# Kernel optimization log

Hardware: AMD Instinct MI355X
Metric: run time of the kernel (lower is better)

Reference implementation:

```python
import jax, jax.numpy as jnp
import numpy as np

TEMPERATURE = 0.1
NEG_FILL = -9e15


def setup_inputs() -> dict:
    key = jax.random.key(0)
    k1, k2, k3, k4 = jax.random.split(key, 4)
    N, D = 2048, 256
    loc1 = jax.random.normal(k1, (N, D), dtype=jnp.float32)
    loc2 = jax.random.normal(k3, (N, D), dtype=jnp.float32)
    # variances must be positive; sample in [0.5, 1.5)
    scale1 = jax.random.uniform(k2, (N, D), dtype=jnp.float32, minval=0.5, maxval=1.5)
    scale2 = jax.random.uniform(k4, (N, D), dtype=jnp.float32, minval=0.5, maxval=1.5)
    return {"loc1": loc1, "scale1": scale1, "loc2": loc2, "scale2": scale2}


def _kl_loss(loc1, scale1, loc2, scale2):
    N, D = loc1.shape
    mu = jnp.concatenate([loc1, loc2], axis=0)    # [2N, D]
    var = jnp.concatenate([scale1, scale2], axis=0)  # [2N, D] (treated as variance)
    inv_var = 1.0 / var
    s_logvar = jnp.sum(jnp.log(var), axis=-1)      # [2N]
    # kld[i,j] = 0.5 * sum_d( logvar_j - logvar_i - 1 + ((mu_i-mu_j)^2 + var_i)/var_j )
    # expand (mu_i-mu_j)^2 = mu_i^2 - 2 mu_i mu_j + mu_j^2 -> three GEMM/reduction terms
    a = (mu * mu + var) @ inv_var.T                # [2N,2N]: sum_d (mu_i^2+var_i)/var_j
    b = mu @ (mu * inv_var).T                      # [2N,2N]: sum_d mu_i mu_j / var_j
    c = jnp.sum(mu * mu * inv_var, axis=-1)        # [2N]:    sum_d mu_j^2 / var_j
    kld = 0.5 * (s_logvar[None, :] - s_logvar[:, None]
                 - jnp.float32(D) + a - 2.0 * b + c[None, :])
    M = 2 * N
    idx = jnp.arange(M)
    kld = kld.at[idx, idx].set(NEG_FILL)           # fill_diagonal_(-9e15)
    sim = kld / TEMPERATURE
    pos = sim[idx, (idx - N) % M]                  # eye rolled by N along dim 0
    loss = jax.nn.logsumexp(sim, axis=-1) - pos
    return jnp.mean(loss)


def reference(loc1, scale1, loc2, scale2):
    return _kl_loss(loc1, scale1, loc2, scale2)
```

## Files before the change

kernel.cpp:

```cpp
#include <hip/hip_runtime.h>
#include <hip/hip_bf16.h>
#include <math.h>

#define N_HALF 2048
#define M_TOT  4096
#define D_DIM  256
#define K2     512
#define NBLK   16
#define NKT    16
#define A_TB   8192
#define B_TB   16384
#define BUF_B  24576
#define NROWB  32

typedef __attribute__((ext_vector_type(8))) short bf16x8;
typedef __attribute__((ext_vector_type(4))) float f32x4;

static __device__ __forceinline__ unsigned short f2bf(float x) {
    union { __hip_bfloat16 h; unsigned short u; } cv;
    cv.h = __float2bfloat16(x);
    return cv.u;
}

static __device__ __forceinline__ void gll16(const void* g, void* l) {
    __builtin_amdgcn_global_load_lds(
        (const __attribute__((address_space(1))) unsigned int*)g,
        (__attribute__((address_space(3))) unsigned int*)l, 16, 0, 0);
}

#define FENCE asm volatile("" ::: "memory")
#define BAR() do { FENCE; __builtin_amdgcn_s_barrier(); FENCE; } while (0)
#define VM(n) asm volatile("s_waitcnt vmcnt(" #n ")" ::: "memory")

__global__ __launch_bounds__(256) void prep_kernel(
        const float* __restrict__ loc1, const float* __restrict__ scale1,
        const float* __restrict__ loc2, const float* __restrict__ scale2,
        unsigned short* __restrict__ Ab, unsigned short* __restrict__ Bb,
        float* __restrict__ slv, float* __restrict__ cvec,
        float* __restrict__ out) {
    const int t = threadIdx.x, w = t >> 6, lane = t & 63;
    if (blockIdx.x == 0 && t == 0) out[0] = 0.0f;
    const int i = blockIdx.x * 4 + w;
    const float* mup  = (i < N_HALF) ? loc1 + (size_t)i * D_DIM   : loc2 + (size_t)(i - N_HALF) * D_DIM;
    const float* vap  = (i < N_HALF) ? scale1 + (size_t)i * D_DIM : scale2 + (size_t)(i - N_HALF) * D_DIM;
    const float4 mu = *(const float4*)(mup + lane * 4);
    const float4 va = *(const float4*)(vap + lane * 4);
    const float4 iv = {1.0f / va.x, 1.0f / va.y, 1.0f / va.z, 1.0f / va.w};

    float lacc = __logf(va.x * va.y * va.z * va.w);
    float cacc = mu.x * mu.x * iv.x + mu.y * mu.y * iv.y
               + mu.z * mu.z * iv.z + mu.w * mu.w * iv.w;
    #pragma unroll
    for (int off = 1; off < 64; off <<= 1) {
        lacc += __shfl_xor(lacc, off, 64);
        cacc += __shfl_xor(cacc, off, 64);
    }
    if (lane == 0) { slv[i] = lacc; cvec[i] = cacc; }

    const int rsw = (i >> 1) & 3;
    char* const abase = (char*)Ab + (size_t)(i >> 7) * (NKT * A_TB) + (i & 127) * 64;
    char* const bbase = (char*)Bb + (size_t)(i >> 8) * (NKT * B_TB) + (i & 255) * 64;
    #define ST4(base, TB, k, v0, v1, v2, v3)                                         \
        {   const int kk = (k);                                                      \
            const int kt = kk >> 5;                                                  \
            const int sl = ((kk >> 3) & 3) ^ rsw, hf = (kk >> 2) & 1;                \
            ushort4 pk = {f2bf(v0), f2bf(v1), f2bf(v2), f2bf(v3)};                   \
            *(ushort4*)((base) + (size_t)kt * (TB) + sl * 16 + hf * 8) = pk; }
    ST4(abase, A_TB, lane * 4,       mu.x * mu.x + va.x, mu.y * mu.y + va.y,
                                     mu.z * mu.z + va.z, mu.w * mu.w + va.w)
    ST4(abase, A_TB, 256 + lane * 4, -2.0f * mu.x, -2.0f * mu.y, -2.0f * mu.z, -2.0f * mu.w)
    ST4(bbase, B_TB, lane * 4,       iv.x, iv.y, iv.z, iv.w)
    ST4(bbase, B_TB, 256 + lane * 4, mu.x * iv.x, mu.y * iv.y, mu.z * iv.z, mu.w * iv.w)
    #undef ST4
}

__global__ __launch_bounds__(512, 4) void gemm_lse_kernel(
        const unsigned short* __restrict__ Ab, const unsigned short* __restrict__ Bb,
        const float* __restrict__ slv, const float* __restrict__ cvec,
        float* __restrict__ pm, float* __restrict__ ps,
        float* __restrict__ pos) {
    extern __shared__ __align__(16) char smem[];
    const int t = threadIdx.x;
    const int lane = t & 63, wid = t >> 6;
    const int bid = blockIdx.x;
    const int xcd = bid & 7, idx = bid >> 3;
    const int by2 = (xcd >> 1) * 8 + (idx >> 3);
    const int bx  = (xcd & 1) * 8 + (idx & 7);
    const int wrow = wid >> 2, wcol = wid & 3;
    const int fr = lane & 15, g = lane >> 4;
    const int t16 = t * 16;

    int a_off[4], b_off[4];
    #pragma unroll
    for (int fm = 0; fm < 4; ++fm) {
        const int row = wrow * 64 + fm * 16 + fr;
        a_off[fm] = row * 64 + ((g ^ ((row >> 1) & 3)) << 4);
    }
    #pragma unroll
    for (int fn = 0; fn < 4; ++fn) {
        const int row = wcol * 64 + fn * 16 + fr;
        b_off[fn] = 8192 + row * 64 + ((g ^ ((row >> 1) & 3)) << 4);
    }

    f32x4 acc[4][4];
    #pragma unroll
    for (int i = 0; i < 4; ++i)
        #pragma unroll
        for (int j = 0; j < 4; ++j) acc[i][j] = (f32x4){0.f, 0.f, 0.f, 0.f};

    const char* gA = (const char*)Ab + (size_t)by2 * (NKT * A_TB);
    const char* gB = (const char*)Bb + (size_t)bx * (NKT * B_TB);

    #define STAGE(ktile, bidx)                                                       \
        {   const char* _sA = gA + (size_t)(ktile) * A_TB;                           \
            const char* _sB = gB + (size_t)(ktile) * B_TB;                           \
            char* _d = smem + (bidx) * BUF_B;                                        \
            gll16(_sA + t16,        _d + t16);                                       \
            gll16(_sB + t16,        _d + 8192 + t16);                                \
            gll16(_sB + 8192 + t16, _d + 16384 + t16); }

    STAGE(0, 0)
    STAGE(1, 1)
    VM(3);
    BAR();

    int cur = 0;
    bf16x8 bfr[4], af[4];
    for (int kt = 0; kt < NKT; ++kt) {
        const char* bufc = smem + cur * BUF_B;
        int stg = cur + 2; if (stg >= 3) stg -= 3;
        if (kt + 2 < NKT) STAGE(kt + 2, stg)
        #pragma unroll
        for (int q = 0; q < 4; ++q) bfr[q] = *(const bf16x8*)(bufc + b_off[q]);
        #pragma unroll
        for (int q = 0; q < 4; ++q) af[q]  = *(const bf16x8*)(bufc + a_off[q]);
        __builtin_amdgcn_s_setprio(1);
        #pragma unroll
        for (int fm = 0; fm < 4; ++fm) {
            acc[fm][0] = __builtin_amdgcn_mfma_f32_16x16x32_bf16(af[fm], bfr[0], acc[fm][0], 0, 0, 0);
            acc[fm][1] = __builtin_amdgcn_mfma_f32_16x16x32_bf16(af[fm], bfr[1], acc[fm][1], 0, 0, 0);
            acc[fm][2] = __builtin_amdgcn_mfma_f32_16x16x32_bf16(af[fm], bfr[2], acc[fm][2], 0, 0, 0);
            acc[fm][3] = __builtin_amdgcn_mfma_f32_16x16x32_bf16(af[fm], bfr[3], acc[fm][3], 0, 0, 0);
        }
        __builtin_amdgcn_s_setprio(0);
        if (kt + 2 < NKT)       { VM(3); }
        else if (kt == NKT - 2) { VM(0); }
        BAR();
        cur = (cur + 1 == 3) ? 0 : cur + 1;
    }
    #undef STAGE

    float colv[4]; int gcol[4];
    #pragma unroll
    for (int fn = 0; fn < 4; ++fn) {
        const int c = bx * 256 + wcol * 64 + fn * 16 + fr;
        gcol[fn] = c;
        colv[fn] = 5.0f * (slv[c] + cvec[c]) - 1280.0f;
    }
    float* redm = (float*)smem;
    float* reds = (float*)(smem + 2048);

    #pragma unroll
    for (int fm = 0; fm < 4; ++fm) {
        #pragma unroll
        for (int q = 0; q < 4; ++q) {
            const int rloc = wrow * 64 + fm * 16 + g * 4 + q;
            const int grow = by2 * 128 + rloc;
            const int jpart = grow ^ N_HALF;
            float v[4];
            #pragma unroll
            for (int fn = 0; fn < 4; ++fn) {
                const float x = 5.0f * acc[fm][fn][q] + colv[fn];
                if (gcol[fn] == jpart) pos[grow] = x;
                v[fn] = (grow == gcol[fn]) ? -3.0e38f : x;
            }
            float m = fmaxf(fmaxf(v[0], v[1]), fmaxf(v[2], v[3]));
            #pragma unroll
            for (int off = 1; off < 16; off <<= 1) m = fmaxf(m, __shfl_xor(m, off, 64));
            float s = __expf(v[0] - m) + __expf(v[1] - m) + __expf(v[2] - m) + __expf(v[3] - m);
            #pragma unroll
            for (int off = 1; off < 16; off <<= 1) s += __shfl_xor(s, off, 64);
            if (fr == 0) { redm[rloc * 4 + wcol] = m; reds[rloc * 4 + wcol] = s; }
        }
    }
    __syncthreads();
    if (t < 128) {
        float m = redm[t * 4], s = reds[t * 4];
        #pragma unroll
        for (int k = 1; k < 4; ++k) {
            const float mk = redm[t * 4 + k], sk = reds[t * 4 + k];
            const float nm = fmaxf(m, mk);
            s = s * __expf(m - nm) + sk * __expf(mk - nm);
            m = nm;
        }
        pm[(size_t)(by2 * 128 + t) * NBLK + bx] = m;
        ps[(size_t)(by2 * 128 + t) * NBLK + bx] = s;
    }
}

__global__ __launch_bounds__(256) void finalize_kernel(
        const float* __restrict__ pm, const float* __restrict__ ps,
        const float* __restrict__ pos, float* __restrict__ out) {
    __shared__ float sm[256];
    const int t = threadIdx.x;
    const int i = blockIdx.x * 256 + t;
    float mk[NBLK];
    float m = -3.0e38f;
    #pragma unroll
    for (int k = 0; k < NBLK; ++k) {
        mk[k] = pm[(size_t)i * NBLK + k];
        m = fmaxf(m, mk[k]);
    }
    float s = 0.0f;
    #pragma unroll
    for (int k = 0; k < NBLK; ++k)
        s += ps[(size_t)i * NBLK + k] * __expf(mk[k] - m);
    sm[t] = m + logf(s) - pos[i];
    __syncthreads();
    for (int off = 128; off > 0; off >>= 1) {
        if (t < off) sm[t] += sm[t + off];
        __syncthreads();
    }
    if (t == 0) atomicAdd(out, sm[0] * (1.0f / (float)M_TOT));
}

extern "C" void kernel_launch(void* const* d_in, const int* in_sizes, int n_in,
                              void* d_out, int out_size, void* d_ws, size_t ws_size,
                              hipStream_t stream) {
    const float* loc1   = (const float*)d_in[0];
    const float* scale1 = (const float*)d_in[1];
    const float* loc2   = (const float*)d_in[2];
    const float* scale2 = (const float*)d_in[3];
    float* out = (float*)d_out;

    char* ws = (char*)d_ws;
    unsigned short* Ab = (unsigned short*)ws;
    unsigned short* Bb = (unsigned short*)(ws + (size_t)4 * 1024 * 1024);
    float* slv  = (float*)(ws + (size_t)8 * 1024 * 1024);
    float* cvec = slv + M_TOT;
    float* pm   = cvec + M_TOT;
    float* ps   = pm + (size_t)M_TOT * NBLK;
    float* pos  = ps + (size_t)M_TOT * NBLK;

    hipLaunchKernelGGL(prep_kernel, dim3(M_TOT / 4), dim3(256), 0, stream,
                       loc1, scale1, loc2, scale2, Ab, Bb, slv, cvec, out);
    hipLaunchKernelGGL(gemm_lse_kernel, dim3(NROWB * NBLK), dim3(512), 73728, stream,
                       Ab, Bb, slv, cvec, pm, ps, pos);
    hipLaunchKernelGGL(finalize_kernel, dim3(NBLK), dim3(256), 0, stream,
                       pm, ps, pos, out);
}
```

Measured before the change: 38.93 us.

## Load A operand directly from global into registers, bypassing LDS staging

Only the B tile is now staged through LDS with the triple-buffered async global-to-LDS copies. Each wave reads its A fragments straight from global memory into registers, and the A layout in the prep kernel becomes unswizzled to match. This cuts LDS traffic and the shared-memory footprint from 72KB to 48KB. The A loads are issued in the same iteration that consumes them, so their global or L2 latency sits directly in front of the MFMAs with no prefetch. Waves that share the same rows also load A redundantly.

Measured after the change: 43.37 us. +11.4%, slower.

```diff
diff --git a/kernel.cpp b/kernel.cpp
--- a/kernel.cpp
+++ b/kernel.cpp
@@ -10,7 +10,7 @@
 #define NKT    16
 #define A_TB   8192
 #define B_TB   16384
-#define BUF_B  24576
+#define BBUF   16384
 #define NROWB  32
 
 typedef __attribute__((ext_vector_type(8))) short bf16x8;
@@ -60,17 +60,17 @@
     const int rsw = (i >> 1) & 3;
     char* const abase = (char*)Ab + (size_t)(i >> 7) * (NKT * A_TB) + (i & 127) * 64;
     char* const bbase = (char*)Bb + (size_t)(i >> 8) * (NKT * B_TB) + (i & 255) * 64;
-    #define ST4(base, TB, k, v0, v1, v2, v3)                                         \
+    #define ST4(base, TB, k, SWZ, v0, v1, v2, v3)                                    \
         {   const int kk = (k);                                                      \
             const int kt = kk >> 5;                                                  \
-            const int sl = ((kk >> 3) & 3) ^ rsw, hf = (kk >> 2) & 1;                \
+            const int sl = ((kk >> 3) & 3) ^ (SWZ), hf = (kk >> 2) & 1;              \
             ushort4 pk = {f2bf(v0), f2bf(v1), f2bf(v2), f2bf(v3)};                   \
             *(ushort4*)((base) + (size_t)kt * (TB) + sl * 16 + hf * 8) = pk; }
-    ST4(abase, A_TB, lane * 4,       mu.x * mu.x + va.x, mu.y * mu.y + va.y,
-                                     mu.z * mu.z + va.z, mu.w * mu.w + va.w)
-    ST4(abase, A_TB, 256 + lane * 4, -2.0f * mu.x, -2.0f * mu.y, -2.0f * mu.z, -2.0f * mu.w)
-    ST4(bbase, B_TB, lane * 4,       iv.x, iv.y, iv.z, iv.w)
-    ST4(bbase, B_TB, 256 + lane * 4, mu.x * iv.x, mu.y * iv.y, mu.z * iv.z, mu.w * iv.w)
+    ST4(abase, A_TB, lane * 4,       0,   mu.x * mu.x + va.x, mu.y * mu.y + va.y,
+                                          mu.z * mu.z + va.z, mu.w * mu.w + va.w)
+    ST4(abase, A_TB, 256 + lane * 4, 0,   -2.0f * mu.x, -2.0f * mu.y, -2.0f * mu.z, -2.0f * mu.w)
+    ST4(bbase, B_TB, lane * 4,       rsw, iv.x, iv.y, iv.z, iv.w)
+    ST4(bbase, B_TB, 256 + lane * 4, rsw, mu.x * iv.x, mu.y * iv.y, mu.z * iv.z, mu.w * iv.w)
     #undef ST4
 }
 
@@ -90,16 +90,11 @@
     const int fr = lane & 15, g = lane >> 4;
     const int t16 = t * 16;
 
-    int a_off[4], b_off[4];
-    #pragma unroll
-    for (int fm = 0; fm < 4; ++fm) {
-        const int row = wrow * 64 + fm * 16 + fr;
-        a_off[fm] = row * 64 + ((g ^ ((row >> 1) & 3)) << 4);
-    }
+    int b_off[4];
     #pragma unroll
     for (int fn = 0; fn < 4; ++fn) {
         const int row = wcol * 64 + fn * 16 + fr;
-        b_off[fn] = 8192 + row * 64 + ((g ^ ((row >> 1) & 3)) << 4);
+        b_off[fn] = row * 64 + ((g ^ ((row >> 1) & 3)) << 4);
     }
 
     f32x4 acc[4][4];
@@ -108,32 +103,31 @@
         #pragma unroll
         for (int j = 0; j < 4; ++j) acc[i][j] = (f32x4){0.f, 0.f, 0.f, 0.f};
 
-    const char* gA = (const char*)Ab + (size_t)by2 * (NKT * A_TB);
+    const char* aPtr = (const char*)Ab + (size_t)by2 * (NKT * A_TB)
+                       + (wrow * 64 + fr) * 64 + g * 16;
     const char* gB = (const char*)Bb + (size_t)bx * (NKT * B_TB);
 
-    #define STAGE(ktile, bidx)                                                       \
-        {   const char* _sA = gA + (size_t)(ktile) * A_TB;                           \
-            const char* _sB = gB + (size_t)(ktile) * B_TB;                           \
-            char* _d = smem + (bidx) * BUF_B;                                        \
-            gll16(_sA + t16,        _d + t16);                                       \
-            gll16(_sB + t16,        _d + 8192 + t16);                                \
-            gll16(_sB + 8192 + t16, _d + 16384 + t16); }
-
-    STAGE(0, 0)
-    STAGE(1, 1)
-    VM(3);
+    #define STAGEB(ktile, bidx)                                                      \
+        {   const char* _sB = gB + (size_t)(ktile) * B_TB;                           \
+            char* _d = smem + (bidx) * BBUF;                                         \
+            gll16(_sB + t16,        _d + t16);                                       \
+            gll16(_sB + 8192 + t16, _d + 8192 + t16); }
+
+    STAGEB(0, 0)
+    STAGEB(1, 1)
+    VM(2);
     BAR();
 
     int cur = 0;
     bf16x8 bfr[4], af[4];
     for (int kt = 0; kt < NKT; ++kt) {
-        const char* bufc = smem + cur * BUF_B;
+        const char* bufc = smem + cur * BBUF;
+        #pragma unroll
+        for (int q = 0; q < 4; ++q) af[q] = *(const bf16x8*)(aPtr + q * 1024);
+        #pragma unroll
+        for (int q = 0; q < 4; ++q) bfr[q] = *(const bf16x8*)(bufc + b_off[q]);
         int stg = cur + 2; if (stg >= 3) stg -= 3;
-        if (kt + 2 < NKT) STAGE(kt + 2, stg)
-        #pragma unroll
-        for (int q = 0; q < 4; ++q) bfr[q] = *(const bf16x8*)(bufc + b_off[q]);
-        #pragma unroll
-        for (int q = 0; q < 4; ++q) af[q]  = *(const bf16x8*)(bufc + a_off[q]);
+        if (kt + 2 < NKT) STAGEB(kt + 2, stg)
         __builtin_amdgcn_s_setprio(1);
         #pragma unroll
         for (int fm = 0; fm < 4; ++fm) {
@@ -143,12 +137,12 @@
             acc[fm][3] = __builtin_amdgcn_mfma_f32_16x16x32_bf16(af[fm], bfr[3], acc[fm][3], 0, 0, 0);
         }
         __builtin_amdgcn_s_setprio(0);
-        if (kt + 2 < NKT)       { VM(3); }
-        else if (kt == NKT - 2) { VM(0); }
+        VM(2);
         BAR();
+        aPtr += A_TB;
         cur = (cur + 1 == 3) ? 0 : cur + 1;
     }
-    #undef STAGE
+    #undef STAGEB
 
     float colv[4]; int gcol[4];
     #pragma unroll
@@ -244,7 +238,7 @@
 
     hipLaunchKernelGGL(prep_kernel, dim3(M_TOT / 4), dim3(256), 0, stream,
                        loc1, scale1, loc2, scale2, Ab, Bb, slv, cvec, out);
-    hipLaunchKernelGGL(gemm_lse_kernel, dim3(NROWB * NBLK), dim3(512), 73728, stream,
+    hipLaunchKernelGGL(gemm_lse_kernel, dim3(NROWB * NBLK), dim3(512), 49152, stream,
                        Ab, Bb, slv, cvec, pm, ps, pos);
     hipLaunchKernelGGL(finalize_kernel, dim3(NBLK), dim3(256), 0, stream,
                        pm, ps, pos, out);
```
